# Optimization experiments

Measured on AMD Instinct MI355X. Metric: run time of the kernel, lower is better.

The kernel has to match this reference:

```python
import jax, jax.numpy as jnp
import numpy as np

B, N, D, H, S = 64, 1000, 512, 8, 20
DK = D // H
TANH_CLIP = 10.0
NEG = -1e9


def setup_inputs() -> dict:
    key = jax.random.key(0)
    k1, k2, k3, k4, k5 = jax.random.split(key, 5)
    embeddings = jax.random.normal(k1, (B, N, D), dtype=jnp.float32)
    q = jax.random.normal(k2, (B, S, D), dtype=jnp.float32)
    # action_mask: True = feasible. Ensure at least one feasible node per row.
    action_mask = jax.random.bernoulli(k3, 0.5, (B, S, N))
    action_mask = action_mask.at[:, :, 0].set(True)
    W_kvl = jax.random.normal(k4, (D, 3 * D), dtype=jnp.float32) * (1.0 / np.sqrt(D))
    W_out = jax.random.normal(k5, (D, D), dtype=jnp.float32) * (1.0 / np.sqrt(D))
    return {"embeddings": embeddings, "q": q, "action_mask": action_mask,
            "W_kvl": W_kvl, "W_out": W_out}


def reference(embeddings, q, action_mask, W_kvl, W_out):
    # _precompute: project node embeddings into glimpse K, V and logit K
    kvl = jnp.einsum('bnd,de->bne', embeddings, W_kvl)  # [B,N,3D]
    glimpse_k, glimpse_v, logit_k = jnp.split(kvl, 3, axis=-1)
    # dynamic embedding is zero (StaticEmbedding for TSP)

    mask = ~action_mask  # True = infeasible, shape [B,S,N]

    # multi-head glimpse attention
    qh = q.reshape(B, S, H, DK)
    kh = glimpse_k.reshape(B, N, H, DK)
    vh = glimpse_v.reshape(B, N, H, DK)
    compat = jnp.einsum('bshd,bnhd->bhsn', qh, kh) / np.sqrt(DK)
    compat = jnp.where(mask[:, None, :, :], NEG, compat)
    attn = jax.nn.softmax(compat, axis=-1)
    heads = jnp.einsum('bhsn,bnhd->bshd', attn, vh).reshape(B, S, D)
    glimpse = jnp.einsum('bsd,de->bse', heads, W_out)  # [B,S,D]

    # pointer logits against logit_k, tanh clipping, mask, log-softmax
    logits = jnp.einsum('bsd,bnd->bsn', glimpse, logit_k) / np.sqrt(D)
    logits = TANH_CLIP * jnp.tanh(logits)
    logits = jnp.where(mask, NEG, logits)
    log_p = jax.nn.log_softmax(logits, axis=-1)  # [B,S,N]

    # rearrange 'b s l -> (s b) l'
    return jnp.swapaxes(log_p, 0, 1).reshape(S * B, N)
```

## Files before the change

kernel.cpp:

```cpp
#include <hip/hip_runtime.h>

#define BB 64
#define NN 1000
#define NP 1024
#define DD 512
#define HH 8
#define SS 20
#define NEGV -1e9f

typedef float v4f __attribute__((ext_vector_type(4)));
typedef short v8s __attribute__((ext_vector_type(8)));
typedef int   v8i __attribute__((ext_vector_type(8)));
typedef int   v4i __attribute__((ext_vector_type(4)));
typedef unsigned char uchar;
typedef unsigned long long ulong_t;

static __device__ __forceinline__ short f2bf(float f) {
    unsigned u = __builtin_bit_cast(unsigned, f);
    u = (u + 0x7fffu + ((u >> 16) & 1u)) >> 16;
    return (short)u;
}
static __device__ __forceinline__ float bf2f(short s) {
    unsigned u = ((unsigned)(unsigned short)s) << 16;
    return __builtin_bit_cast(float, u);
}
static __device__ __forceinline__ uchar f2fp8(float f) {
    return (uchar)(__builtin_amdgcn_cvt_pk_fp8_f32(f, 0.f, 0, false) & 0xff);
}

static __device__ __forceinline__ void gld16(const void* g, void* l) {
    __builtin_amdgcn_global_load_lds(
        (const __attribute__((address_space(1))) void*)(g),
        (__attribute__((address_space(3))) void*)(l),
        16, 0, 0);
}

__global__ void prep(const float* __restrict__ Wkvl, uchar* __restrict__ Wt8,
                     const float* __restrict__ Wout, short* __restrict__ Wot,
                     const float* __restrict__ emb, int* __restrict__ emb8) {
    __shared__ float t[32][33];
    int bid = blockIdx.x, tid = threadIdx.x;
    if (bid < 768) {
        int c0 = (bid % 48) * 32, r0 = (bid / 48) * 32;
        int x = tid & 31, y = tid >> 5;
        for (int k = 0; k < 32; k += 8)
            t[y + k][x] = Wkvl[(long)(r0 + y + k) * 1536 + c0 + x];
        __syncthreads();
        for (int k = 0; k < 32; k += 8)
            Wt8[(long)(c0 + y + k) * 512 + r0 + x] = f2fp8(t[x][y + k]);
    } else if (bid < 1024) {
        int bb = bid - 768;
        int c0 = (bb & 15) * 32, r0 = (bb >> 4) * 32;
        int x = tid & 31, y = tid >> 5;
        for (int k = 0; k < 32; k += 8)
            t[y + k][x] = Wout[(long)(r0 + y + k) * 512 + c0 + x];
        __syncthreads();
        for (int k = 0; k < 32; k += 8)
            Wot[(long)(c0 + y + k) * 512 + r0 + x] = f2bf(t[x][y + k]);
    } else {
        int i = (bid - 1024) * 256 + tid;
        long o = (long)i * 8;
        v4f a = *(const v4f*)(emb + o);
        v4f b = *(const v4f*)(emb + o + 4);
        int lo = __builtin_amdgcn_cvt_pk_fp8_f32(a.x, a.y, 0, false);
        lo = __builtin_amdgcn_cvt_pk_fp8_f32(a.z, a.w, lo, true);
        int hi = __builtin_amdgcn_cvt_pk_fp8_f32(b.x, b.y, 0, false);
        hi = __builtin_amdgcn_cvt_pk_fp8_f32(b.z, b.w, hi, true);
        int2 r; r.x = lo; r.y = hi;
        *(int2*)(emb8 + i * 2) = r;
    }
}

__global__ __launch_bounds__(512, 2) void gemm_kvl(const uchar* __restrict__ emb8,
                                                   const uchar* __restrict__ Wt8,
                                                   uchar* __restrict__ kvl8) {
    extern __shared__ __align__(16) uchar smem[];
    uchar* As0 = smem;
    uchar* Bs0 = smem + 65536;
    int tid = threadIdx.x;
    int id = blockIdx.x;
    int xcd = id & 7, j0 = id >> 3;
    int wgid = (xcd < 4 ? xcd * 188 : 752 + (xcd - 4) * 187) + j0;
    int m_idx = wgid / 6, n_idx = wgid - m_idx * 6;
    int m0 = m_idx * 256, n0 = n_idx * 256;
    int wid = tid >> 6, lane = tid & 63, quad = lane >> 4, l16 = lane & 15;
    int wm = wid & 1, wn = wid >> 1;
    const uchar* Ag = emb8 + (long)m0 * 512;
    const uchar* Bg = Wt8 + (long)n0 * 512;
    int rsub = lane >> 3;
    int kc = ((lane & 7) ^ rsub) * 16;

    v4f acc[8][4] = {};

    auto stage2 = [&](int bi, int kk, int p) {
        int rl = wid * 32 + p * 8;
        gld16(Ag + (long)(rl + rsub) * 512 + kk + kc, As0 + bi * 32768 + rl * 128);
        gld16(Bg + (long)(rl + rsub) * 512 + kk + kc, Bs0 + bi * 32768 + rl * 128);
    };
    auto ldfrag = [&](const uchar* base, int row) -> v8i {
        int c0 = (quad * 2) ^ (row & 7);
        v4i lo = *(const v4i*)(base + row * 128 + c0 * 16);
        v4i hi = *(const v4i*)(base + row * 128 + (c0 ^ 1) * 16);
        return __builtin_shufflevector(lo, hi, 0, 1, 2, 3, 4, 5, 6, 7);
    };

    #pragma unroll
    for (int p = 0; p < 4; ++p) stage2(0, 0, p);
    __syncthreads();

    v8i af[4], bf[4];
    for (int t = 0; t < 4; ++t) {
        int cur = t & 1;
        const uchar* ab = As0 + cur * 32768;
        const uchar* bb = Bs0 + cur * 32768;
        int kn = (t + 1) * 128;
        #pragma unroll
        for (int i = 0; i < 4; ++i) af[i] = ldfrag(ab, wm * 128 + i * 16 + l16);
        #pragma unroll
        for (int jj = 0; jj < 2; ++jj) bf[jj] = ldfrag(bb, wn * 64 + jj * 16 + l16);
        if (t < 3) stage2(cur ^ 1, kn, 0);
        __builtin_amdgcn_s_barrier();
        __builtin_amdgcn_s_setprio(1);
        #pragma unroll
        for (int i = 0; i < 4; ++i)
            #pragma unroll
            for (int jj = 0; jj < 2; ++jj)
                acc[i][jj] = __builtin_amdgcn_mfma_scale_f32_16x16x128_f8f6f4(
                    af[i], bf[jj], acc[i][jj], 0, 0, 0, 0x7f7f7f7f, 0, 0x7f7f7f7f);
        __builtin_amdgcn_s_setprio(0);
        __builtin_amdgcn_s_barrier();
        #pragma unroll
        for (int jj = 2; jj < 4; ++jj) bf[jj] = ldfrag(bb, wn * 64 + jj * 16 + l16);
        if (t < 3) stage2(cur ^ 1, kn, 1);
        __builtin_amdgcn_s_barrier();
        __builtin_amdgcn_s_setprio(1);
        #pragma unroll
        for (int i = 0; i < 4; ++i)
            #pragma unroll
            for (int jj = 2; jj < 4; ++jj)
                acc[i][jj] = __builtin_amdgcn_mfma_scale_f32_16x16x128_f8f6f4(
                    af[i], bf[jj], acc[i][jj], 0, 0, 0, 0x7f7f7f7f, 0, 0x7f7f7f7f);
        __builtin_amdgcn_s_setprio(0);
        __builtin_amdgcn_s_barrier();
        #pragma unroll
        for (int i = 0; i < 4; ++i) af[i] = ldfrag(ab, wm * 128 + (i + 4) * 16 + l16);
        if (t < 3) stage2(cur ^ 1, kn, 2);
        __builtin_amdgcn_s_barrier();
        __builtin_amdgcn_s_setprio(1);
        #pragma unroll
        for (int i = 0; i < 4; ++i)
            #pragma unroll
            for (int jj = 0; jj < 2; ++jj)
                acc[i + 4][jj] = __builtin_amdgcn_mfma_scale_f32_16x16x128_f8f6f4(
                    af[i], bf[jj], acc[i + 4][jj], 0, 0, 0, 0x7f7f7f7f, 0, 0x7f7f7f7f);
        __builtin_amdgcn_s_setprio(0);
        __builtin_amdgcn_s_barrier();
        if (t < 3) stage2(cur ^ 1, kn, 3);
        __builtin_amdgcn_s_barrier();
        __builtin_amdgcn_s_setprio(1);
        #pragma unroll
        for (int i = 0; i < 4; ++i)
            #pragma unroll
            for (int jj = 2; jj < 4; ++jj)
                acc[i + 4][jj] = __builtin_amdgcn_mfma_scale_f32_16x16x128_f8f6f4(
                    af[i], bf[jj], acc[i + 4][jj], 0, 0, 0, 0x7f7f7f7f, 0, 0x7f7f7f7f);
        __builtin_amdgcn_s_setprio(0);
        __syncthreads();
    }

    short* rp = (short*)smem;
    short* r = rp + wid * (16 * 72);
    #pragma unroll
    for (int i = 0; i < 8; ++i) {
        #pragma unroll
        for (int jj = 0; jj < 4; ++jj)
            #pragma unroll
            for (int rr = 0; rr < 4; ++rr)
                r[(quad * 4 + rr) * 72 + jj * 16 + l16] = f2bf(acc[i][jj][rr]);
        #pragma unroll
        for (int h = 0; h < 2; ++h) {
            int rowl = h * 8 + (lane >> 3);
            int colc = (lane & 7) * 8;
            v8s val = *(const v8s*)(r + rowl * 72 + colc);
            int lo = __builtin_amdgcn_cvt_pk_fp8_f32(bf2f(val[0]), bf2f(val[1]), 0, false);
            lo = __builtin_amdgcn_cvt_pk_fp8_f32(bf2f(val[2]), bf2f(val[3]), lo, true);
            int hi = __builtin_amdgcn_cvt_pk_fp8_f32(bf2f(val[4]), bf2f(val[5]), 0, false);
            hi = __builtin_amdgcn_cvt_pk_fp8_f32(bf2f(val[6]), bf2f(val[7]), hi, true);
            int2 st; st.x = lo; st.y = hi;
            *(int2*)(kvl8 + (long)(m0 + wm * 128 + i * 16 + rowl) * 1536 +
                     n0 + wn * 64 + colc) = st;
        }
    }
}

__global__ void transpose_v(const uchar* __restrict__ kvl8, uchar* __restrict__ Vt8) {
    int bh = blockIdx.x, b = bh >> 3, h = bh & 7;
    int n0 = blockIdx.y * 64;
    __shared__ uchar T[64][72];
    int tid = threadIdx.x;
    #pragma unroll
    for (int it = 0; it < 2; ++it) {
        int nl = (tid >> 3) + it * 32;
        int n = n0 + nl;
        int nc = n < NN ? n : NN - 1;
        int d0 = (tid & 7) * 8;
        ulong_t v = *(const ulong_t*)(kvl8 + ((long)b * NN + nc) * 1536 + DD + h * 64 + d0);
        uchar* vb = (uchar*)&v;
        #pragma unroll
        for (int j = 0; j < 8; ++j) T[d0 + j][nl] = vb[j];
    }
    __syncthreads();
    #pragma unroll
    for (int it = 0; it < 2; ++it) {
        int d = (tid >> 3) + it * 32;
        int ns = (tid & 7) * 8;
        *(ulong_t*)(Vt8 + ((long)bh * 64 + d) * NP + n0 + ns) = *(const ulong_t*)&T[d][ns];
    }
}

#define CST 1036
__global__ __launch_bounds__(512) void attn_fused(const float* __restrict__ q,
                                                  const uchar* __restrict__ kvl8,
                                                  const uchar* __restrict__ Vt8,
                                                  const int* __restrict__ mask,
                                                  float* __restrict__ heads) {
    int b = blockIdx.x, h = blockIdx.y;
    __shared__ __align__(16) uchar qs[32 * 72];
    __shared__ __align__(16) short cmp[SS * CST];
    int tid = threadIdx.x, wid = tid >> 6, lane = tid & 63, quad = lane >> 4, l16 = lane & 15;
    for (int i = tid; i < 32 * 64; i += 512) {
        int row = i >> 6, col = i & 63;
        float v = (row < SS) ? q[((long)b * SS + row) * DD + h * 64 + col] : 0.f;
        qs[row * 72 + col] = f2fp8(v);
    }
    __syncthreads();
    long af[2][2];
    #pragma unroll
    for (int mt = 0; mt < 2; ++mt)
        #pragma unroll
        for (int ks = 0; ks < 2; ++ks)
            af[mt][ks] = *(const long*)(qs + (mt * 16 + l16) * 72 + ks * 32 + quad * 8);
    for (int t = 0; t < 8; ++t) {
        int nt = wid * 8 + t;
        int n = nt * 16 + l16;
        int nc = n < NN ? n : NN - 1;
        const uchar* kp = kvl8 + ((long)b * NN + nc) * 1536 + h * 64 + quad * 8;
        long b0 = *(const long*)kp;
        long b1 = *(const long*)(kp + 32);
        #pragma unroll
        for (int mt = 0; mt < 2; ++mt) {
            v4f a = {};
            a = __builtin_amdgcn_mfma_f32_16x16x32_fp8_fp8(af[mt][0], b0, a, 0, 0, 0);
            a = __builtin_amdgcn_mfma_f32_16x16x32_fp8_fp8(af[mt][1], b1, a, 0, 0, 0);
            #pragma unroll
            for (int r = 0; r < 4; ++r) {
                int s = mt * 16 + quad * 4 + r;
                if (s < SS) cmp[s * CST + nt * 16 + l16] = f2bf(a[r] * 0.125f);
            }
        }
    }
    __syncthreads();
    for (int s = wid; s < SS; s += 8) {
        const int* mr = mask + ((long)b * SS + s) * NN;
        float x[16];
        float mx = NEGV;
        #pragma unroll
        for (int i = 0; i < 16; ++i) {
            int n = lane + 64 * i;
            float v = bf2f(cmp[s * CST + n]);
            bool feas = (n < NN) && (mr[n < NN ? n : 0] != 0);
            x[i] = feas ? v : NEGV;
            mx = fmaxf(mx, x[i]);
        }
        for (int off = 32; off; off >>= 1) mx = fmaxf(mx, __shfl_xor(mx, off));
        float sum = 0.f;
        #pragma unroll
        for (int i = 0; i < 16; ++i) { x[i] = __expf(x[i] - mx); sum += x[i]; }
        for (int off = 32; off; off >>= 1) sum += __shfl_xor(sum, off);
        float inv = 1.0f / sum;
        uchar* pr = (uchar*)cmp + (long)s * (CST * 2);
        #pragma unroll
        for (int i = 0; i < 16; ++i) pr[lane + 64 * i] = f2fp8(x[i] * inv);
    }
    __syncthreads();
    int mt = wid & 1, dt = wid >> 1;
    int srow = mt * 16 + l16; if (srow > SS - 1) srow = SS - 1;
    const uchar* ap = (const uchar*)cmp + (long)srow * (CST * 2) + quad * 8;
    const uchar* vb = Vt8 + (long)(b * HH + h) * 64 * NP;
    v4f acc = {};
    for (int k0 = 0; k0 < NP; k0 += 32) {
        long afr = *(const long*)(ap + k0);
        long bfr = *(const long*)(vb + (long)(dt * 16 + l16) * NP + k0 + quad * 8);
        acc = __builtin_amdgcn_mfma_f32_16x16x32_fp8_fp8(afr, bfr, acc, 0, 0, 0);
    }
    #pragma unroll
    for (int r = 0; r < 4; ++r) {
        int s = mt * 16 + quad * 4 + r;
        if (s < SS)
            heads[((long)b * SS + s) * DD + h * 64 + dt * 16 + l16] = acc[r];
    }
}

__global__ __launch_bounds__(256) void out_proj(const float* __restrict__ heads,
                                                const short* __restrict__ Wot,
                                                float* __restrict__ glimpse) {
    __shared__ __align__(16) short As[64 * 40], Bs[64 * 40];
    int tid = threadIdx.x;
    int m0 = blockIdx.x * 64, n0 = blockIdx.y * 64;
    int wid = tid >> 6, lane = tid & 63, quad = lane >> 4, l16 = lane & 15;
    int wm = wid & 1, wn = wid >> 1;
    int arow = tid >> 3, akol = (tid & 7) * 4;
    int brow = tid >> 2, bkol = (tid & 3) * 8;
    v4f acc[2][2] = {};
    for (int kk = 0; kk < 512; kk += 32) {
        #pragma unroll
        for (int p = 0; p < 2; ++p) {
            int r = arow + p * 32;
            v4f a = *(const v4f*)(heads + (long)(m0 + r) * 512 + kk + akol);
            short4 s4;
            s4.x = f2bf(a.x); s4.y = f2bf(a.y); s4.z = f2bf(a.z); s4.w = f2bf(a.w);
            *(short4*)(As + r * 40 + akol) = s4;
        }
        *(uint4*)(Bs + brow * 40 + bkol) =
            *(const uint4*)(Wot + (long)(n0 + brow) * 512 + kk + bkol);
        __syncthreads();
        #pragma unroll
        for (int i = 0; i < 2; ++i) {
            v8s af = *(const v8s*)(As + (wm * 32 + i * 16 + l16) * 40 + quad * 8);
            #pragma unroll
            for (int j = 0; j < 2; ++j) {
                v8s bf = *(const v8s*)(Bs + (wn * 32 + j * 16 + l16) * 40 + quad * 8);
                acc[i][j] = __builtin_amdgcn_mfma_f32_16x16x32_bf16(af, bf, acc[i][j], 0, 0, 0);
            }
        }
        __syncthreads();
    }
    #pragma unroll
    for (int i = 0; i < 2; ++i)
        #pragma unroll
        for (int j = 0; j < 2; ++j)
            #pragma unroll
            for (int r = 0; r < 4; ++r)
                glimpse[(long)(m0 + wm * 32 + i * 16 + quad * 4 + r) * 512 +
                        n0 + wn * 32 + j * 16 + l16] = acc[i][j][r];
}

__global__ __launch_bounds__(256) void ptr_logits(const float* __restrict__ glimpse,
                                                  const uchar* __restrict__ kvl8,
                                                  float* __restrict__ logits) {
    int b = blockIdx.x, g = blockIdx.y;
    __shared__ __align__(16) uchar Gs[32 * 520];
    int tid = threadIdx.x;
    #pragma unroll
    for (int it = 0; it < 16; ++it) {
        int e = it * 1024 + tid * 4;
        int row = e >> 9, col = e & 511;
        int pk = 0;
        if (row < SS) {
            v4f a = *(const v4f*)(glimpse + ((long)b * SS + row) * 512 + col);
            pk = __builtin_amdgcn_cvt_pk_fp8_f32(a.x, a.y, 0, false);
            pk = __builtin_amdgcn_cvt_pk_fp8_f32(a.z, a.w, pk, true);
        }
        *(int*)(Gs + row * 520 + col) = pk;
    }
    __syncthreads();
    int wid = tid >> 6, lane = tid & 63, quad = lane >> 4, l16 = lane & 15;
    const float scale = 0.04419417382415922f;
    int nt = g * 4 + wid;
    int n = nt * 16 + l16;
    int ncl = n < NN ? n : NN - 1;
    const uchar* kp = kvl8 + ((long)b * NN + ncl) * 1536 + 1024 + quad * 8;
    v4f acc[2] = {};
    for (int k = 0; k < 16; ++k) {
        long bfr = *(const long*)(kp + k * 32);
        #pragma unroll
        for (int m = 0; m < 2; ++m) {
            long afr = *(const long*)(Gs + (m * 16 + l16) * 520 + k * 32 + quad * 8);
            acc[m] = __builtin_amdgcn_mfma_f32_16x16x32_fp8_fp8(afr, bfr, acc[m], 0, 0, 0);
        }
    }
    #pragma unroll
    for (int m = 0; m < 2; ++m)
        #pragma unroll
        for (int r = 0; r < 4; ++r) {
            int s = m * 16 + quad * 4 + r;
            if (s < SS)
                logits[((long)b * SS + s) * NP + nt * 16 + l16] = acc[m][r] * scale;
        }
}

__global__ __launch_bounds__(256) void logsoftmax_out(const float* __restrict__ logits,
                                                      const int* __restrict__ mask,
                                                      float* __restrict__ out) {
    int row = blockIdx.x;
    int b = row / SS, s = row % SS;
    int tid = threadIdx.x;
    __shared__ float red[8];
    int n0 = tid * 4;
    v4f v = *(const v4f*)(logits + (long)row * NP + n0);
    const int* mr = mask + (long)row * NN;
    float x[4];
    float mx = NEGV;
    #pragma unroll
    for (int j = 0; j < 4; ++j) {
        int n = n0 + j;
        float t = 10.f * tanhf(v[j]);
        bool feas = (n < NN) && (mr[n < NN ? n : 0] != 0);
        x[j] = feas ? t : NEGV;
        mx = fmaxf(mx, x[j]);
    }
    for (int off = 32; off; off >>= 1) mx = fmaxf(mx, __shfl_xor(mx, off));
    int wid = tid >> 6, lane = tid & 63;
    if (lane == 0) red[wid] = mx;
    __syncthreads();
    mx = fmaxf(fmaxf(red[0], red[1]), fmaxf(red[2], red[3]));
    float sum = 0.f;
    #pragma unroll
    for (int j = 0; j < 4; ++j) sum += __expf(x[j] - mx);
    for (int off = 32; off; off >>= 1) sum += __shfl_xor(sum, off);
    __syncthreads();
    if (lane == 0) red[4 + wid] = sum;
    __syncthreads();
    sum = red[4] + red[5] + red[6] + red[7];
    float lse = mx + __logf(sum);
    float* orow = out + ((long)s * BB + b) * NN;
    #pragma unroll
    for (int j = 0; j < 4; ++j) {
        int n = n0 + j;
        if (n < NN) orow[n] = x[j] - lse;
    }
}

extern "C" void kernel_launch(void* const* d_in, const int* in_sizes, int n_in,
                              void* d_out, int out_size, void* d_ws, size_t ws_size,
                              hipStream_t stream) {
    const float* emb  = (const float*)d_in[0];
    const float* q    = (const float*)d_in[1];
    const int*   mask = (const int*)d_in[2];
    const float* Wkvl = (const float*)d_in[3];
    const float* Wout = (const float*)d_in[4];
    float* out = (float*)d_out;

    char* ws = (char*)d_ws;
    uchar* kvl8    = (uchar*)ws; ws += (size_t)64000 * 1536;
    uchar* Vt8     = (uchar*)ws; ws += (size_t)512 * 64 * NP;
    uchar* Wt8     = (uchar*)ws; ws += (size_t)1536 * 512;
    uchar* emb8    = (uchar*)ws; ws += (size_t)64000 * 512;
    short* Wot     = (short*)ws; ws += (size_t)512 * 512 * 2;
    float* heads   = (float*)ws; ws += (size_t)BB * SS * DD * 4;
    float* glimpse = (float*)ws; ws += (size_t)BB * SS * DD * 4;
    float* logits  = (float*)ws; ws += (size_t)BB * SS * NP * 4;

    static int s_attr_done = 0;
    if (!s_attr_done) {
        hipFuncSetAttribute(reinterpret_cast<const void*>(gemm_kvl),
                            hipFuncAttributeMaxDynamicSharedMemorySize, 131072);
        s_attr_done = 1;
    }

    prep<<<dim3(1024 + 16000), 256, 0, stream>>>(Wkvl, Wt8, Wout, Wot, emb, (int*)emb8);
    gemm_kvl<<<dim3(1500), 512, 131072, stream>>>(emb8, Wt8, kvl8);
    transpose_v<<<dim3(512, 16), 256, 0, stream>>>(kvl8, Vt8);
    attn_fused<<<dim3(BB, HH), 512, 0, stream>>>(q, kvl8, Vt8, mask, heads);
    out_proj<<<dim3(20, 8), 256, 0, stream>>>(heads, Wot, glimpse);
    ptr_logits<<<dim3(BB, 16), 256, 0, stream>>>(glimpse, kvl8, logits);
    logsoftmax_out<<<dim3(BB * SS), 256, 0, stream>>>(logits, mask, out);
}
```

Before: 361.0 us.

## Prefetch two K-tiles ahead in FP8 projection GEMM with vmcnt-based waits

Restructures the FP8 projection GEMM's global-to-LDS staging so both buffers are filled up front, and the next-next K tile is loaded into the current buffer after its last fragment reads. Full __syncthreads per iteration are replaced by explicit vmcnt waits plus barriers, and the K loop is fully unrolled. This is meant to give global loads more time in flight and to drop one barrier per iteration. It relies on correct vmcnt accounting and risks write-after-read hazards on the reused LDS buffer.

Measured after the change: 346.4 us. -4.1%, faster.

```diff
diff --git a/kernel.cpp b/kernel.cpp
--- a/kernel.cpp
+++ b/kernel.cpp
@@ -92,10 +92,19 @@
 
     v4f acc[8][4] = {};
 
-    auto stage2 = [&](int bi, int kk, int p) {
-        int rl = wid * 32 + p * 8;
-        gld16(Ag + (long)(rl + rsub) * 512 + kk + kc, As0 + bi * 32768 + rl * 128);
-        gld16(Bg + (long)(rl + rsub) * 512 + kk + kc, Bs0 + bi * 32768 + rl * 128);
+    auto stageA = [&](int bi, int kk) {
+        #pragma unroll
+        for (int p = 0; p < 4; ++p) {
+            int rl = wid * 32 + p * 8;
+            gld16(Ag + (long)(rl + rsub) * 512 + kk + kc, As0 + bi * 32768 + rl * 128);
+        }
+    };
+    auto stageB = [&](int bi, int kk) {
+        #pragma unroll
+        for (int p = 0; p < 4; ++p) {
+            int rl = wid * 32 + p * 8;
+            gld16(Bg + (long)(rl + rsub) * 512 + kk + kc, Bs0 + bi * 32768 + rl * 128);
+        }
     };
     auto ldfrag = [&](const uchar* base, int row) -> v8i {
         int c0 = (quad * 2) ^ (row & 7);
@@ -104,21 +113,23 @@
         return __builtin_shufflevector(lo, hi, 0, 1, 2, 3, 4, 5, 6, 7);
     };
 
-    #pragma unroll
-    for (int p = 0; p < 4; ++p) stage2(0, 0, p);
-    __syncthreads();
+    stageA(0, 0); stageB(0, 0);
+    stageA(1, 128); stageB(1, 128);
+    asm volatile("s_waitcnt vmcnt(8)" ::: "memory");
+    __builtin_amdgcn_s_barrier();
+    __builtin_amdgcn_sched_barrier(0);
 
     v8i af[4], bf[4];
+    #pragma unroll
     for (int t = 0; t < 4; ++t) {
         int cur = t & 1;
         const uchar* ab = As0 + cur * 32768;
         const uchar* bb = Bs0 + cur * 32768;
-        int kn = (t + 1) * 128;
+        int kn2 = (t + 2) * 128;
         #pragma unroll
         for (int i = 0; i < 4; ++i) af[i] = ldfrag(ab, wm * 128 + i * 16 + l16);
         #pragma unroll
         for (int jj = 0; jj < 2; ++jj) bf[jj] = ldfrag(bb, wn * 64 + jj * 16 + l16);
-        if (t < 3) stage2(cur ^ 1, kn, 0);
         __builtin_amdgcn_s_barrier();
         __builtin_amdgcn_s_setprio(1);
         #pragma unroll
@@ -131,7 +142,6 @@
         __builtin_amdgcn_s_barrier();
         #pragma unroll
         for (int jj = 2; jj < 4; ++jj) bf[jj] = ldfrag(bb, wn * 64 + jj * 16 + l16);
-        if (t < 3) stage2(cur ^ 1, kn, 1);
         __builtin_amdgcn_s_barrier();
         __builtin_amdgcn_s_setprio(1);
         #pragma unroll
@@ -144,7 +154,7 @@
         __builtin_amdgcn_s_barrier();
         #pragma unroll
         for (int i = 0; i < 4; ++i) af[i] = ldfrag(ab, wm * 128 + (i + 4) * 16 + l16);
-        if (t < 3) stage2(cur ^ 1, kn, 2);
+        if (t < 2) stageB(cur, kn2);
         __builtin_amdgcn_s_barrier();
         __builtin_amdgcn_s_setprio(1);
         #pragma unroll
@@ -155,8 +165,7 @@
                     af[i], bf[jj], acc[i + 4][jj], 0, 0, 0, 0x7f7f7f7f, 0, 0x7f7f7f7f);
         __builtin_amdgcn_s_setprio(0);
         __builtin_amdgcn_s_barrier();
-        if (t < 3) stage2(cur ^ 1, kn, 3);
-        __builtin_amdgcn_s_barrier();
+        if (t < 2) stageA(cur, kn2);
         __builtin_amdgcn_s_setprio(1);
         #pragma unroll
         for (int i = 0; i < 4; ++i)
@@ -165,8 +174,14 @@
                 acc[i + 4][jj] = __builtin_amdgcn_mfma_scale_f32_16x16x128_f8f6f4(
                     af[i], bf[jj], acc[i + 4][jj], 0, 0, 0, 0x7f7f7f7f, 0, 0x7f7f7f7f);
         __builtin_amdgcn_s_setprio(0);
-        __syncthreads();
-    }
+        if (t < 3) {
+            if (t < 2) asm volatile("s_waitcnt vmcnt(8)" ::: "memory");
+            else       asm volatile("s_waitcnt vmcnt(0)" ::: "memory");
+            __builtin_amdgcn_s_barrier();
+            __builtin_amdgcn_sched_barrier(0);
+        }
+    }
+    __syncthreads();
 
     short* rp = (short*)smem;
     short* r = rp + wid * (16 * 72);
```
